# Kernel tuning notes

Hardware: AMD Instinct MI355X
Metric: run time of the kernel (lower is better)

The kernel has to match this reference:

```python
import jax, jax.numpy as jnp
import numpy as np
from jax.scipy.special import digamma

T, K, D = 8192, 64, 128


def setup_inputs() -> dict:
    key = jax.random.key(0)
    ks = jax.random.split(key, 7)
    mu_t = jax.random.normal(ks[0], (T, D), jnp.float32)
    diag_var_t = jax.random.uniform(ks[1], (T, D), jnp.float32)  # encoder diag variances >= 0
    niw_mu = jax.random.normal(ks[2], (K, D), jnp.float32)
    A = jax.random.normal(ks[3], (K, D, D), jnp.float32) / np.sqrt(D)
    niw_Psi = jnp.einsum('kde,kfe->kdf', A, A) + float(D) * jnp.eye(D, dtype=jnp.float32)[None]  # SPD
    niw_nu = D + 2.0 + 10.0 * jax.random.uniform(ks[4], (K,), jnp.float32)  # nu > D+1
    phi = 0.1 + 4.0 * jax.random.uniform(ks[5], (K, K), jnp.float32)  # Dirichlet posterior params > 0
    log_pi = jax.nn.log_softmax(jax.random.normal(ks[6], (K,), jnp.float32))
    return dict(mu_t=mu_t, diag_var_t=diag_var_t, niw_mu=niw_mu, niw_Psi=niw_Psi,
                niw_nu=niw_nu, phi=phi, log_pi=log_pi)


def _emission_logB(mu_t, diag_var_t, niw_mu, niw_Psi, niw_nu):
    # E[Lambda_k] = nu_k * Psi_k^{-1}; E[log|Lambda_k|] via multivariate digamma
    L = jnp.linalg.cholesky(niw_Psi)                                  # [K,D,D]
    logdet_Psi = 2.0 * jnp.sum(jnp.log(jnp.diagonal(L, axis1=-2, axis2=-1)), axis=-1)  # [K]
    eye = jnp.broadcast_to(jnp.eye(D, dtype=niw_Psi.dtype), (K, D, D))
    Psi_inv = jax.scipy.linalg.cho_solve((L, True), eye)              # [K,D,D]
    E_Lam = niw_nu[:, None, None] * Psi_inv                           # [K,D,D]
    i = jnp.arange(1, D + 1, dtype=niw_Psi.dtype)[None, :]            # [1,D]
    E_logdet = jnp.sum(digamma((niw_nu[:, None] + 1.0 - i) / 2.0), axis=1) \
        + D * jnp.log(jnp.asarray(2.0, niw_Psi.dtype)) - logdet_Psi   # [K]
    diagv = jnp.clip(diag_var_t, 0.0)                                 # [T,D]
    diff = mu_t[:, None, :] - niw_mu[None, :, :]                      # [T,K,D]
    quad_mean = jnp.einsum('tkd,kde,tke->tk', diff, E_Lam, diff)      # [T,K]
    ELam_diag = jnp.diagonal(E_Lam, axis1=-2, axis2=-1)               # [K,D]
    trace_diag = jnp.einsum('td,kd->tk', diagv, ELam_diag)            # [T,K]
    const = -0.5 * D * jnp.log(jnp.asarray(2.0 * np.pi, mu_t.dtype))
    return 0.5 * E_logdet[None, :] + const - 0.5 * (quad_mean + trace_diag)


def _forward_backward(log_pi, ElogA, logB):
    a0 = log_pi + logB[0]
    z0 = jax.nn.logsumexp(a0)
    alpha0 = a0 - z0

    def fwd_step(aprev, logb):
        pred = jax.nn.logsumexp(aprev[:, None] + ElogA, axis=0)
        a = pred + logb
        z = jax.nn.logsumexp(a)
        return a - z, (a - z, z)

    _, (alpha_rest, z_rest) = jax.lax.scan(fwd_step, alpha0, logB[1:])
    alpha = jnp.concatenate([alpha0[None], alpha_rest], axis=0)       # [T,K]
    logZ = jnp.concatenate([z0[None], z_rest], axis=0)                # [T]

    def bwd_step(bnext, xs):
        logb_next, z_next = xs
        b = jax.nn.logsumexp(ElogA + (logb_next + bnext)[None, :], axis=1) - z_next
        return b, b

    beta_T = jnp.zeros_like(alpha0)
    _, beta_rest = jax.lax.scan(bwd_step, beta_T, (logB[1:], logZ[1:]), reverse=True)
    beta = jnp.concatenate([beta_rest, beta_T[None]], axis=0)         # [T,K]

    rhat_log = alpha + beta
    rhat_log = rhat_log - jax.nn.logsumexp(rhat_log, axis=1, keepdims=True)
    rhat = jnp.exp(rhat_log)

    x = alpha[:-1, :, None] + ElogA[None, :, :] + (logB[1:] + beta[1:])[:, None, :]  # [T-1,K,K]
    x = x - jax.nn.logsumexp(x.reshape(x.shape[0], -1), axis=1)[:, None, None]
    xihat = jnp.exp(x)

    ll = jnp.sum(logZ)
    return rhat, xihat, ll


def reference(mu_t, diag_var_t, niw_mu, niw_Psi, niw_nu, phi, log_pi):
    logB = _emission_logB(mu_t, diag_var_t, niw_mu, niw_Psi, niw_nu)  # [T,K]
    ElogA = digamma(phi) - digamma(jnp.sum(phi, axis=1, keepdims=True))  # [K,K]
    rhat, xihat, ll = _forward_backward(log_pi, ElogA, logB)
    return rhat, xihat, ll
```

## Files before the change

kernel.cpp:

```cpp
#include <hip/hip_runtime.h>
#include <math.h>

#define T_LEN 8192
#define KK 64
#define DD 128
#define RS 132
#define GP 68

typedef __bf16  bf16x4 __attribute__((ext_vector_type(4)));
typedef __bf16  bf16x8 __attribute__((ext_vector_type(8)));
typedef float  f32x16 __attribute__((ext_vector_type(16)));

__device__ __forceinline__ float wred_max(float v){
#pragma unroll
  for (int m = 1; m < 64; m <<= 1) v = fmaxf(v, __shfl_xor(v, m, 64));
  return v;
}
__device__ __forceinline__ float wred_sum(float v){
#pragma unroll
  for (int m = 1; m < 64; m <<= 1) v += __shfl_xor(v, m, 64);
  return v;
}
__device__ __forceinline__ float digamma_f(float x){
  float r = 0.f;
  while (x < 6.f){ r -= 1.f/x; x += 1.f; }
  float ix = 1.f/x, ix2 = ix*ix;
  return r + logf(x) - 0.5f*ix - ix2*(0.0833333333f - ix2*(0.0083333333f - ix2*0.0039682540f));
}

__global__ void __launch_bounds__(256, 1) k_neumann(
    const float* __restrict__ Psi, const float* __restrict__ niw_mu,
    const float* __restrict__ nu_, const float* __restrict__ phi,
    __bf16* __restrict__ Ebf, float* __restrict__ EdiagT,
    float* __restrict__ cvecT, float* __restrict__ rK, float* __restrict__ Lhalf,
    float* __restrict__ sclK,
    float* __restrict__ ElogA, float* __restrict__ P, float* __restrict__ PT)
{
  extern __shared__ float lds[];
  float* Rl = lds;
  float* Pb = lds + DD*RS;
  __shared__ float red[256];
  __shared__ float msh[DD];
  int k = blockIdx.x, tid = threadIdx.x;
  const float* A = Psi + (size_t)k*DD*DD;

  if (tid < 64){
    float ph = phi[k*KK + tid];
    float s  = wred_sum(ph);
    float e  = digamma_f(ph) - digamma_f(s);
    ElogA[k*KK + tid] = e;
    float p = expf(e);
    P [k*KK + tid] = p;
    PT[tid*KK + k] = p;
  }

  float tl = 0.f;
  for (int d = tid; d < DD; d += 256) tl += A[d*DD + d];
  red[tid] = tl; __syncthreads();
  for (int off = 128; off > 0; off >>= 1){ if (tid < off) red[tid] += red[tid+off]; __syncthreads(); }
  float c = red[0] / (float)DD;
  __syncthreads();

  float trpow = 0.f;
  for (int idx = tid; idx < DD*DD; idx += 256){
    int d = idx >> 7, e = idx & 127;
    float v = ((d == e) ? 1.f : 0.f) - A[idx]/c;
    Rl[d*RS + e] = v;
    if (d == e) trpow += v;
  }
  __syncthreads();

  int tr = tid >> 4, tc = tid & 15;
  int r0 = tr*8, c0 = tc*8;
  float S[8][8];
#pragma unroll
  for (int i = 0; i < 8; i++)
#pragma unroll
    for (int j = 0; j < 8; j++){
      float v = Rl[(r0+i)*RS + c0+j];
      if (r0+i == c0+j) v += 1.f;
      S[i][j] = v;
    }

  {
    float Cc[8][8];
#pragma unroll
    for (int i = 0; i < 8; i++)
#pragma unroll
      for (int j = 0; j < 8; j++) Cc[i][j] = 0.f;
    for (int l = 0; l < DD; l += 4){
      float af[4][8], bf[4][8];
#pragma unroll
      for (int q = 0; q < 4; q++){
        float4 x0 = *(const float4*)&Rl[(l+q)*RS + r0];
        float4 x1 = *(const float4*)&Rl[(l+q)*RS + r0 + 4];
        af[q][0]=x0.x; af[q][1]=x0.y; af[q][2]=x0.z; af[q][3]=x0.w;
        af[q][4]=x1.x; af[q][5]=x1.y; af[q][6]=x1.z; af[q][7]=x1.w;
        float4 y0 = *(const float4*)&Rl[(l+q)*RS + c0];
        float4 y1 = *(const float4*)&Rl[(l+q)*RS + c0 + 4];
        bf[q][0]=y0.x; bf[q][1]=y0.y; bf[q][2]=y0.z; bf[q][3]=y0.w;
        bf[q][4]=y1.x; bf[q][5]=y1.y; bf[q][6]=y1.z; bf[q][7]=y1.w;
      }
#pragma unroll
      for (int q = 0; q < 4; q++)
#pragma unroll
        for (int i = 0; i < 8; i++)
#pragma unroll
          for (int j = 0; j < 8; j++)
            Cc[i][j] = fmaf(af[q][i], bf[q][j], Cc[i][j]);
    }
#pragma unroll
    for (int i = 0; i < 8; i++)
#pragma unroll
      for (int j = 0; j < 8; j++) S[i][j] += Cc[i][j];
    if (tr == tc){
#pragma unroll
      for (int i = 0; i < 8; i++) trpow += Cc[i][i]*0.5f;
    }
  }

  red[tid] = trpow; __syncthreads();
  for (int off = 128; off > 0; off >>= 1){ if (tid < off) red[tid] += red[tid+off]; __syncthreads(); }
  float trsum = red[0];
  __syncthreads();

  float nu = nu_[k];
  float dl = 0.f;
  for (int i = tid; i < DD; i += 256) dl += digamma_f((nu - (float)i)*0.5f);
  red[tid] = dl; __syncthreads();
  for (int off = 128; off > 0; off >>= 1){ if (tid < off) red[tid] += red[tid+off]; __syncthreads(); }
  if (tid == 0){
    float logdetPsi = (float)DD*logf(c) - trsum;
    float Elogdet = red[0] + (float)DD*0.69314718056f - logdetPsi;
    Lhalf[k] = 0.5f*Elogdet - 0.5f*(float)DD*1.83787706641f;
    sclK[k]  = nu / c;
  }
  __syncthreads();

  float scl = nu / c;
#pragma unroll
  for (int i = 0; i < 8; i++)
#pragma unroll
    for (int j = 0; j < 8; j++){
      float sv = S[i][j];
      bool dg = (r0+i == c0+j);
      if (dg) EdiagT[(r0+i)*KK + k] = scl*sv;
      float et = scl*(sv - (dg ? 1.f : 0.f));
      int r = (r0+i)*DD + (c0+j);
      Ebf[(size_t)(r>>4)*1024 + k*16 + (r&15)] = (__bf16)et;
    }
#pragma unroll
  for (int i = 0; i < 8; i++){
    float4 w0, w1;
    w0.x=S[i][0]; w0.y=S[i][1]; w0.z=S[i][2]; w0.w=S[i][3];
    w1.x=S[i][4]; w1.y=S[i][5]; w1.z=S[i][6]; w1.w=S[i][7];
    *(float4*)&Pb[(r0+i)*RS + c0]     = w0;
    *(float4*)&Pb[(r0+i)*RS + c0 + 4] = w1;
  }
  for (int d = tid; d < DD; d += 256) msh[d] = niw_mu[k*DD + d];
  __syncthreads();
  float cv = 0.f;
  if (tid < DD){
    float acc = 0.f;
    for (int e = 0; e < DD; e++) acc += Pb[tid*RS + e]*msh[e];
    cv = scl*acc;
    cvecT[tid*KK + k] = cv;
  }
  red[tid] = (tid < DD) ? msh[tid]*cv : 0.f; __syncthreads();
  for (int off = 128; off > 0; off >>= 1){ if (tid < off) red[tid] += red[tid+off]; __syncthreads(); }
  if (tid == 0) rK[k] = red[0];
}

__global__ void __launch_bounds__(256, 1) k_q1(const float* __restrict__ mu,
      const __bf16* __restrict__ Ebf, float* __restrict__ part)
{
  __shared__ float muF[32*132];
  __shared__ float trb[128*66];
  int b = blockIdx.x;
  int rs = b & 3, tseg = b >> 2;
  int t0 = tseg*128, d0 = rs*32;
  int tid = threadIdx.x;
  int w = tid >> 6, lane = tid & 63;
  int kh = w & 1, th = w >> 1;
  int l31 = lane & 31;
  int k0 = (lane >> 5)*8;

  for (int v = tid; v < 128*32; v += 256){
    int t = v >> 5, d = v & 31;
    muF[d*132 + t] = mu[(size_t)(t0+t)*DD + d0 + d];
  }

  bf16x8 Bf0[8], Bf1[8];
#pragma unroll
  for (int c = 0; c < 8; c++){
    int tc0 = t0 + th*64 + l31;
    int tc1 = tc0 + 32;
    float4 x0 = *(const float4*)&mu[(size_t)tc0*DD + c*16 + k0];
    float4 x1 = *(const float4*)&mu[(size_t)tc0*DD + c*16 + k0 + 4];
    bf16x8 hv;
    hv[0]=(__bf16)x0.x; hv[1]=(__bf16)x0.y; hv[2]=(__bf16)x0.z; hv[3]=(__bf16)x0.w;
    hv[4]=(__bf16)x1.x; hv[5]=(__bf16)x1.y; hv[6]=(__bf16)x1.z; hv[7]=(__bf16)x1.w;
    Bf0[c] = hv;
    float4 y0 = *(const float4*)&mu[(size_t)tc1*DD + c*16 + k0];
    float4 y1 = *(const float4*)&mu[(size_t)tc1*DD + c*16 + k0 + 4];
    bf16x8 gv;
    gv[0]=(__bf16)y0.x; gv[1]=(__bf16)y0.y; gv[2]=(__bf16)y0.z; gv[3]=(__bf16)y0.w;
    gv[4]=(__bf16)y1.x; gv[5]=(__bf16)y1.y; gv[6]=(__bf16)y1.z; gv[7]=(__bf16)y1.w;
    Bf1[c] = gv;
  }
  __syncthreads();

  const unsigned short* __restrict__ Eu = (const unsigned short*)Ebf;
  size_t abase = (size_t)(kh*32 + l31)*16 + k0;

  f32x16 acc0, acc1;
#pragma unroll
  for (int i = 0; i < 16; i++){ acc0[i]=0.f; acc1[i]=0.f; }

  uint4 A0[8], A1[8];
  {
    const unsigned short* ap = Eu + (size_t)d0*8192 + abase;
#pragma unroll
    for (int c = 0; c < 8; c++) A0[c] = *(const uint4*)(ap + c*1024);
#pragma unroll
    for (int c = 0; c < 8; c++) A1[c] = *(const uint4*)(ap + 8192 + c*1024);
  }

  for (int dd = 0; dd < 32; dd += 2){
    {
      f32x16 ta, tb;
#pragma unroll
      for (int i = 0; i < 16; i++){ ta[i]=0.f; tb[i]=0.f; }
#pragma unroll
      for (int c = 0; c < 8; c++){
        bf16x8 av = *(bf16x8*)&A0[c];
        ta = __builtin_amdgcn_mfma_f32_32x32x16_bf16(av, Bf0[c], ta, 0, 0, 0);
        tb = __builtin_amdgcn_mfma_f32_32x32x16_bf16(av, Bf1[c], tb, 0, 0, 0);
      }
      float m0 = muF[dd*132 + th*64 + l31];
      float m1 = muF[dd*132 + th*64 + 32 + l31];
#pragma unroll
      for (int i = 0; i < 16; i++){
        acc0[i] = fmaf(m0, ta[i], acc0[i]);
        acc1[i] = fmaf(m1, tb[i], acc1[i]);
      }
    }
    if (dd + 2 < 32){
      const unsigned short* ap = Eu + (size_t)(d0+dd+2)*8192 + abase;
#pragma unroll
      for (int c = 0; c < 8; c++) A0[c] = *(const uint4*)(ap + c*1024);
    }
    {
      f32x16 ta, tb;
#pragma unroll
      for (int i = 0; i < 16; i++){ ta[i]=0.f; tb[i]=0.f; }
#pragma unroll
      for (int c = 0; c < 8; c++){
        bf16x8 av = *(bf16x8*)&A1[c];
        ta = __builtin_amdgcn_mfma_f32_32x32x16_bf16(av, Bf0[c], ta, 0, 0, 0);
        tb = __builtin_amdgcn_mfma_f32_32x32x16_bf16(av, Bf1[c], tb, 0, 0, 0);
      }
      float m0 = muF[(dd+1)*132 + th*64 + l31];
      float m1 = muF[(dd+1)*132 + th*64 + 32 + l31];
#pragma unroll
      for (int i = 0; i < 16; i++){
        acc0[i] = fmaf(m0, ta[i], acc0[i]);
        acc1[i] = fmaf(m1, tb[i], acc1[i]);
      }
    }
    if (dd + 3 < 32){
      const unsigned short* ap = Eu + (size_t)(d0+dd+3)*8192 + abase;
#pragma unroll
      for (int c = 0; c < 8; c++) A1[c] = *(const uint4*)(ap + c*1024);
    }
  }

  __syncthreads();
#pragma unroll
  for (int r = 0; r < 16; r++){
    int krow = kh*32 + (r&3) + 8*(r>>2) + 4*(lane>>5);
    trb[(th*64 + l31)*66 + krow]      = acc0[r];
    trb[(th*64 + 32 + l31)*66 + krow] = acc1[r];
  }
  __syncthreads();
  float* dst = part + (size_t)rs*T_LEN*KK;
  {
    int t = tid >> 1, kc = (tid & 1)*32;
#pragma unroll
    for (int q = 0; q < 8; q++){
      float4 vv = *(float4*)&trb[t*66 + kc + q*4];
      *(float4*)&dst[(size_t)(t0+t)*KK + kc + q*4] = vv;
    }
  }
}

__global__ void __launch_bounds__(256) k_logBall(
    const float* __restrict__ part, const float* __restrict__ mu, const float* __restrict__ dvar,
    const float* __restrict__ cvecT, const float* __restrict__ EdiagT,
    const float* __restrict__ rK, const float* __restrict__ Lhalf, const float* __restrict__ sclK,
    float* __restrict__ logB, float* __restrict__ mrow, float* __restrict__ btil)
{
  int tid = threadIdx.x; int k = tid & 63; int w = tid >> 6;
  float rk = rK[k], lh = Lhalf[k], scl = sclK[k];
  int tbase = blockIdx.x*32 + w*8;
  float a1[8], a2[8], ssv[8];
#pragma unroll
  for (int tt = 0; tt < 8; tt++){ a1[tt]=0.f; a2[tt]=0.f; ssv[tt]=0.f; }
  for (int dc = 0; dc < DD; dc += 4){
    float c0 = cvecT[(dc+0)*KK + k], c1 = cvecT[(dc+1)*KK + k];
    float c2 = cvecT[(dc+2)*KK + k], c3 = cvecT[(dc+3)*KK + k];
    float e0 = EdiagT[(dc+0)*KK + k], e1 = EdiagT[(dc+1)*KK + k];
    float e2 = EdiagT[(dc+2)*KK + k], e3 = EdiagT[(dc+3)*KK + k];
#pragma unroll
    for (int tt = 0; tt < 8; tt++){
      float4 m4 = *(const float4*)(mu   + (size_t)(tbase+tt)*DD + dc);
      float4 v4 = *(const float4*)(dvar + (size_t)(tbase+tt)*DD + dc);
      a1[tt] = fmaf(m4.x,c0, fmaf(m4.y,c1, fmaf(m4.z,c2, fmaf(m4.w,c3, a1[tt]))));
      a2[tt] = fmaf(fmaxf(v4.x,0.f),e0, fmaf(fmaxf(v4.y,0.f),e1,
               fmaf(fmaxf(v4.z,0.f),e2, fmaf(fmaxf(v4.w,0.f),e3, a2[tt]))));
      ssv[tt] = fmaf(m4.x,m4.x, fmaf(m4.y,m4.y, fmaf(m4.z,m4.z, fmaf(m4.w,m4.w, ssv[tt]))));
    }
  }
#pragma unroll
  for (int tt = 0; tt < 8; tt++){
    int t = tbase + tt;
    float q = scl*ssv[tt]
            + part[(size_t)0*T_LEN*KK + (size_t)t*KK + k]
            + part[(size_t)1*T_LEN*KK + (size_t)t*KK + k]
            + part[(size_t)2*T_LEN*KK + (size_t)t*KK + k]
            + part[(size_t)3*T_LEN*KK + (size_t)t*KK + k];
    float lb = lh - 0.5f*(q - 2.f*a1[tt] + rk + a2[tt]);
    float m  = wred_max(lb);
    logB[(size_t)t*KK + k] = lb;
    btil[(size_t)t*KK + k] = expf(lb - m);
    if (k == 0) mrow[t] = m;
  }
}

__global__ void __launch_bounds__(128, 1) k_pass1(const float* __restrict__ Pm,
     const float* __restrict__ btil, float* __restrict__ G8)
{
  __shared__ float G[64*GP];
  __shared__ float wmax[2][2];
  int tid = threadIdx.x, w = tid >> 6, lane = tid & 63;
  int chunk = blockIdx.x;
  int kb8 = (lane >> 5)*8;
  int n = lane & 31;

  bf16x8 Bhi[4][2], Blo[4][2];
#pragma unroll
  for (int Kb = 0; Kb < 4; Kb++)
#pragma unroll
    for (int J = 0; J < 2; J++){
#pragma unroll
      for (int j = 0; j < 8; j++){
        float p = Pm[(Kb*16 + kb8 + j)*KK + J*32 + n];
        __bf16 h = (__bf16)p;
        Bhi[Kb][J][j] = h;
        Blo[Kb][J][j] = (__bf16)(p - (float)h);
      }
    }
  for (int v = tid; v < 64*64; v += 128){
    int i = v >> 6, j = v & 63;
    G[i*GP + j] = (i == j) ? 1.f : 0.f;
  }
  __syncthreads();

  int m = w*32 + n;
  for (int s = 0; s < 8; s++){
    int t = chunk*8 + s;
    if (t >= 1){
      f32x16 acc0, acc1;
#pragma unroll
      for (int i = 0; i < 16; i++){ acc0[i] = 0.f; acc1[i] = 0.f; }
#pragma unroll
      for (int Kb = 0; Kb < 4; Kb++){
        float4 x0 = *(const float4*)&G[m*GP + Kb*16 + kb8];
        float4 x1 = *(const float4*)&G[m*GP + Kb*16 + kb8 + 4];
        float xv[8] = {x0.x,x0.y,x0.z,x0.w,x1.x,x1.y,x1.z,x1.w};
        bf16x8 ah, al;
#pragma unroll
        for (int j = 0; j < 8; j++){
          __bf16 h = (__bf16)xv[j];
          ah[j] = h;
          al[j] = (__bf16)(xv[j] - (float)h);
        }
        acc0 = __builtin_amdgcn_mfma_f32_32x32x16_bf16(ah, Bhi[Kb][0], acc0, 0,0,0);
        acc0 = __builtin_amdgcn_mfma_f32_32x32x16_bf16(ah, Blo[Kb][0], acc0, 0,0,0);
        acc0 = __builtin_amdgcn_mfma_f32_32x32x16_bf16(al, Bhi[Kb][0], acc0, 0,0,0);
        acc1 = __builtin_amdgcn_mfma_f32_32x32x16_bf16(ah, Bhi[Kb][1], acc1, 0,0,0);
        acc1 = __builtin_amdgcn_mfma_f32_32x32x16_bf16(ah, Blo[Kb][1], acc1, 0,0,0);
        acc1 = __builtin_amdgcn_mfma_f32_32x32x16_bf16(al, Bhi[Kb][1], acc1, 0,0,0);
      }
      float b0 = btil[(size_t)t*KK + n];
      float b1 = btil[(size_t)t*KK + 32 + n];
      float mx = 0.f;
#pragma unroll
      for (int i = 0; i < 16; i++){
        acc0[i] *= b0; acc1[i] *= b1;
        mx = fmaxf(mx, fmaxf(acc0[i], acc1[i]));
      }
      mx = wred_max(mx);
      if (lane == 0) wmax[s&1][w] = mx;
      __syncthreads();
      float inv = 1.f/fmaxf(wmax[s&1][0], wmax[s&1][1]);
#pragma unroll
      for (int r = 0; r < 16; r++){
        int row = w*32 + (r&3) + 8*(r>>2) + 4*(lane>>5);
        G[row*GP + n]      = acc0[r]*inv;
        G[row*GP + 32 + n] = acc1[r]*inv;
      }
    }
  }
  __syncthreads();
  float* dst = G8 + (size_t)chunk*4096;
  for (int v = tid; v < 4096; v += 128) dst[v] = G[(v>>6)*GP + (v&63)];
}

__device__ void chain_body(const float* __restrict__ s0, int chain,
    float* __restrict__ X, float (*wmax)[2],
    float* __restrict__ dstLin, int tid, int w, int lane)
{
  int kb8 = (lane >> 5)*8;
  int n = lane & 31;
  int m = w*32 + n;

  for (int v = tid; v < 4096; v += 128) X[(v>>6)*GP + (v&63)] = s0[v];
  __syncthreads();

  for (int j = 1; j < chain; j++){
    const float* Y = s0 + (size_t)j*4096;
    bf16x8 Bh[4][2], Bl[4][2];
#pragma unroll
    for (int Kb = 0; Kb < 4; Kb++)
#pragma unroll
      for (int J = 0; J < 2; J++){
#pragma unroll
        for (int jj = 0; jj < 8; jj++){
          float p = Y[(Kb*16 + kb8 + jj)*64 + J*32 + n];
          __bf16 h = (__bf16)p;
          Bh[Kb][J][jj] = h;
          Bl[Kb][J][jj] = (__bf16)(p - (float)h);
        }
      }
    f32x16 acc0, acc1;
#pragma unroll
    for (int i = 0; i < 16; i++){ acc0[i] = 0.f; acc1[i] = 0.f; }
#pragma unroll
    for (int Kb = 0; Kb < 4; Kb++){
      float4 x0 = *(const float4*)&X[m*GP + Kb*16 + kb8];
      float4 x1 = *(const float4*)&X[m*GP + Kb*16 + kb8 + 4];
      float xv[8] = {x0.x,x0.y,x0.z,x0.w,x1.x,x1.y,x1.z,x1.w};
      bf16x8 ah, al;
#pragma unroll
      for (int q = 0; q < 8; q++){
        __bf16 h = (__bf16)xv[q];
        ah[q] = h;
        al[q] = (__bf16)(xv[q] - (float)h);
      }
      acc0 = __builtin_amdgcn_mfma_f32_32x32x16_bf16(ah, Bh[Kb][0], acc0, 0,0,0);
      acc0 = __builtin_amdgcn_mfma_f32_32x32x16_bf16(ah, Bl[Kb][0], acc0, 0,0,0);
      acc0 = __builtin_amdgcn_mfma_f32_32x32x16_bf16(al, Bh[Kb][0], acc0, 0,0,0);
      acc1 = __builtin_amdgcn_mfma_f32_32x32x16_bf16(ah, Bh[Kb][1], acc1, 0,0,0);
      acc1 = __builtin_amdgcn_mfma_f32_32x32x16_bf16(ah, Bl[Kb][1], acc1, 0,0,0);
      acc1 = __builtin_amdgcn_mfma_f32_32x32x16_bf16(al, Bh[Kb][1], acc1, 0,0,0);
    }
    float mx = 0.f;
#pragma unroll
    for (int i = 0; i < 16; i++) mx = fmaxf(mx, fmaxf(acc0[i], acc1[i]));
    mx = wred_max(mx);
    if (lane == 0) wmax[j&1][w] = mx;
    __syncthreads();
    float inv = 1.f/fmaxf(wmax[j&1][0], wmax[j&1][1]);
#pragma unroll
    for (int r = 0; r < 16; r++){
      int row = w*32 + (r&3) + 8*(r>>2) + 4*(lane>>5);
      X[row*GP + n]      = acc0[r]*inv;
      X[row*GP + 32 + n] = acc1[r]*inv;
    }
    __syncthreads();
  }
  for (int v = tid; v < 4096; v += 128) dstLin[v] = X[(v>>6)*GP + (v&63)];
}

__global__ void __launch_bounds__(128, 1) k_chain8(const float* __restrict__ G8,
        float* __restrict__ H64)
{
  __shared__ float X[64*GP];
  __shared__ float wmax[2][2];
  int tid = threadIdx.x, w = tid >> 6, lane = tid & 63;
  int bid = blockIdx.x;
  chain_body(G8 + (size_t)bid*8*4096, 8, X, wmax, H64 + (size_t)bid*4096, tid, w, lane);
}

__device__ void mat_combine(const float* __restrict__ A, const float* __restrict__ B,
    float* __restrict__ out, float* __restrict__ outT,
    float* __restrict__ X, float* __restrict__ wmax, int tid, int w, int lane)
{
  int kb8 = (lane >> 5)*8;
  int n = lane & 31;
  int m = w*32 + n;
  for (int v = tid; v < 4096; v += 128) X[(v>>6)*GP + (v&63)] = A[v];
  bf16x8 Bh[4][2], Bl[4][2];
#pragma unroll
  for (int Kb = 0; Kb < 4; Kb++)
#pragma unroll
    for (int J = 0; J < 2; J++){
#pragma unroll
      for (int jj = 0; jj < 8; jj++){
        float p = B[(Kb*16 + kb8 + jj)*64 + J*32 + n];
        __bf16 h = (__bf16)p;
        Bh[Kb][J][jj] = h;
        Bl[Kb][J][jj] = (__bf16)(p - (float)h);
      }
    }
  __syncthreads();
  f32x16 acc0, acc1;
#pragma unroll
  for (int i = 0; i < 16; i++){ acc0[i] = 0.f; acc1[i] = 0.f; }
#pragma unroll
  for (int Kb = 0; Kb < 4; Kb++){
    float4 x0 = *(const float4*)&X[m*GP + Kb*16 + kb8];
    float4 x1 = *(const float4*)&X[m*GP + Kb*16 + kb8 + 4];
    float xv[8] = {x0.x,x0.y,x0.z,x0.w,x1.x,x1.y,x1.z,x1.w};
    bf16x8 ah, al;
#pragma unroll
    for (int q = 0; q < 8; q++){
      __bf16 h = (__bf16)xv[q];
      ah[q] = h;
      al[q] = (__bf16)(xv[q] - (float)h);
    }
    acc0 = __builtin_amdgcn_mfma_f32_32x32x16_bf16(ah, Bh[Kb][0], acc0, 0,0,0);
    acc0 = __builtin_amdgcn_mfma_f32_32x32x16_bf16(ah, Bl[Kb][0], acc0, 0,0,0);
    acc0 = __builtin_amdgcn_mfma_f32_32x32x16_bf16(al, Bh[Kb][0], acc0, 0,0,0);
    acc1 = __builtin_amdgcn_mfma_f32_32x32x16_bf16(ah, Bh[Kb][1], acc1, 0,0,0);
    acc1 = __builtin_amdgcn_mfma_f32_32x32x16_bf16(ah, Bl[Kb][1], acc1, 0,0,0);
    acc1 = __builtin_amdgcn_mfma_f32_32x32x16_bf16(al, Bh[Kb][1], acc1, 0,0,0);
  }
  float mx = 0.f;
#pragma unroll
  for (int i = 0; i < 16; i++) mx = fmaxf(mx, fmaxf(acc0[i], acc1[i]));
  mx = wred_max(mx);
  if (lane == 0) wmax[w] = mx;
  __syncthreads();
  float inv = 1.f/fmaxf(wmax[0], wmax[1]);
#pragma unroll
  for (int r = 0; r < 16; r++){
    int row = w*32 + (r&3) + 8*(r>>2) + 4*(lane>>5);
    out[row*64 + n]      = acc0[r]*inv;
    out[row*64 + 32 + n] = acc1[r]*inv;
  }
  if (outT){
    __syncthreads();
#pragma unroll
    for (int r = 0; r < 16; r++){
      int row = w*32 + (r&3) + 8*(r>>2) + 4*(lane>>5);
      X[row*GP + n]      = acc0[r]*inv;
      X[row*GP + 32 + n] = acc1[r]*inv;
    }
    __syncthreads();
    for (int v = tid; v < 4096; v += 128) outT[v] = X[(v&63)*GP + (v>>6)];
  }
}

__device__ void mat_copy(const float* __restrict__ A, float* __restrict__ out,
    float* __restrict__ outT, float* __restrict__ X, int tid)
{
  if (!outT){
    for (int v = tid; v < 4096; v += 128) out[v] = A[v];
  } else {
    for (int v = tid; v < 4096; v += 128){
      float vv = A[v];
      out[v] = vv;
      X[(v>>6)*GP + (v&63)] = vv;
    }
    __syncthreads();
    for (int v = tid; v < 4096; v += 128) outT[v] = X[(v&63)*GP + (v>>6)];
  }
}

__global__ void __launch_bounds__(128, 1) k_ks(
    const float* __restrict__ PAin, float* __restrict__ PAout,
    const float* __restrict__ SBin, float* __restrict__ SBout,
    float* __restrict__ SBT, int s, int wrT)
{
  __shared__ float X[64*GP];
  __shared__ float wmax[2];
  int tid = threadIdx.x, w = tid >> 6, lane = tid & 63;
  int c = blockIdx.x;
  if (c >= s)
    mat_combine(PAin + (size_t)(c-s)*4096, PAin + (size_t)c*4096,
                PAout + (size_t)c*4096, nullptr, X, wmax, tid, w, lane);
  else
    mat_copy(PAin + (size_t)c*4096, PAout + (size_t)c*4096, nullptr, X, tid);
  __syncthreads();
  float* t = wrT ? (SBT + (size_t)c*4096) : nullptr;
  if (c + s <= 127)
    mat_combine(SBin + (size_t)c*4096, SBin + (size_t)(c+s)*4096,
                SBout + (size_t)c*4096, t, X, wmax, tid, w, lane);
  else
    mat_copy(SBin + (size_t)c*4096, SBout + (size_t)c*4096, t, X, tid);
}

__global__ void __launch_bounds__(64, 1) k_pass3(const float* __restrict__ Pm, const float* __restrict__ PTm,
   const float* __restrict__ PA, const float* __restrict__ SBT,
   const float* __restrict__ logB, const float* __restrict__ mrow, const float* __restrict__ btil,
   const float* __restrict__ log_pi,
   float* __restrict__ alphahat, float* __restrict__ betahat, float* __restrict__ llpart)
{
  int lane = threadIdx.x;
  int bid = blockIdx.x;
  if (bid < 128){
    int c = bid;
    float Preg[64];
#pragma unroll
    for (int i = 0; i < 64; i++) Preg[i] = Pm[i*64 + lane];
    float a; float llacc = 0.f;
    int tstart;
    float x0v = log_pi[lane] + logB[lane];
    float mm0 = wred_max(x0v);
    float e0 = expf(x0v - mm0);
    float ss0 = wred_sum(e0);
    if (c == 0){
      a = e0/ss0;
      llacc = mm0 + logf(ss0);
      alphahat[lane] = a;
      tstart = 1;
    } else {
      float a0 = e0/ss0;
      const float* H = PA + (size_t)(c-1)*4096;
      float Hr[64];
#pragma unroll
      for (int i = 0; i < 64; i++) Hr[i] = H[i*64 + lane];
      float p0 = 0.f, p1 = 0.f, p2 = 0.f, p3 = 0.f;
#pragma unroll
      for (int i = 0; i < 16; i++){
        p0 = fmaf(__shfl(a0, i,      64), Hr[i],      p0);
        p1 = fmaf(__shfl(a0, i + 16, 64), Hr[i + 16], p1);
        p2 = fmaf(__shfl(a0, i + 32, 64), Hr[i + 32], p2);
        p3 = fmaf(__shfl(a0, i + 48, 64), Hr[i + 48], p3);
      }
      a = (p0 + p1) + (p2 + p3);
      a /= wred_sum(a);
      tstart = c*64;
    }
    int tend = c*64 + 64;
    float bt = btil[(size_t)tstart*KK + lane];
    for (int t = tstart; t < tend; t++){
      float btn = 0.f;
      if (t + 1 < tend) btn = btil[(size_t)(t+1)*KK + lane];
      float mr = mrow[t];
      float p0 = 0.f, p1 = 0.f, p2 = 0.f, p3 = 0.f;
#pragma unroll
      for (int i = 0; i < 16; i++){
        p0 = fmaf(__shfl(a, i,      64), Preg[i],      p0);
        p1 = fmaf(__shfl(a, i + 16, 64), Preg[i + 16], p1);
        p2 = fmaf(__shfl(a, i + 32, 64), Preg[i + 32], p2);
        p3 = fmaf(__shfl(a, i + 48, 64), Preg[i + 48], p3);
      }
      float pred = (p0 + p1) + (p2 + p3);
      a = pred * bt;
      if (((t - tstart) & 3) == 3 || t == tend - 1){
        float s = wred_sum(a);
        a = a / s;
        llacc += logf(s);
      }
      llacc += mr;
      alphahat[(size_t)t*KK + lane] = a;
      bt = btn;
    }
    if (lane == 0) llpart[c] = llacc;
  } else {
    int c = bid - 128;
    float PTreg[64];
#pragma unroll
    for (int j = 0; j < 64; j++) PTreg[j] = PTm[j*64 + lane];
    float b, lb;
    if (c == 127){
      b = 1.f; lb = 0.f;
    } else {
      const float* H = SBT + (size_t)(c+1)*4096;
      float s0 = 0.f, s1 = 0.f, s2 = 0.f, s3 = 0.f;
#pragma unroll
      for (int i = 0; i < 16; i++){
        s0 += H[(i     )*64 + lane];
        s1 += H[(i + 16)*64 + lane];
        s2 += H[(i + 32)*64 + lane];
        s3 += H[(i + 48)*64 + lane];
      }
      float s = (s0 + s1) + (s2 + s3);
      float mmb = wred_max(s);
      b = s/mmb;
      lb = logf(b);
    }
    int t1 = c*64 + 63;
    betahat[(size_t)t1*KK + lane] = b;
    float lgb = logB[(size_t)t1*KK + lane];
    float mrn = mrow[t1];
    for (int t = t1 - 1; t >= c*64; t--){
      float lgbn = 0.f, mrnn = 0.f;
      if (t > c*64){
        lgbn = logB[(size_t)t*KK + lane];
        mrnn = mrow[t];
      }
      float lv = (lgb - mrn) + lb;
      float vm = wred_max(lv);
      float vv = expf(lv - vm);
      float q0 = 0.f, q1r = 0.f, q2 = 0.f, q3 = 0.f;
#pragma unroll
      for (int j = 0; j < 16; j++){
        q0  = fmaf(PTreg[j],      __shfl(vv, j,      64), q0);
        q1r = fmaf(PTreg[j + 16], __shfl(vv, j + 16, 64), q1r);
        q2  = fmaf(PTreg[j + 32], __shfl(vv, j + 32, 64), q2);
        q3  = fmaf(PTreg[j + 48], __shfl(vv, j + 48, 64), q3);
      }
      b = (q0 + q1r) + (q2 + q3);
      lb = logf(b);
      betahat[(size_t)t*KK + lane] = b;
      lgb = lgbn; mrn = mrnn;
    }
  }
}

__global__ void __launch_bounds__(256) k_outs(const float* __restrict__ ah,
     const float* __restrict__ bh, const float* __restrict__ ElogA,
     const float* __restrict__ logB, const float* __restrict__ llp,
     float* __restrict__ out_rhat, float* __restrict__ out_xi, float* __restrict__ out_ll)
{
  __shared__ float la[64], wc[64];
  __shared__ float redm[4], reds[4];
  int tid = threadIdx.x;
  int b = blockIdx.x;
  if (tid < 64) la[tid] = logf(ah[(size_t)b*KK + tid]);
  else if (tid < 128 && b < T_LEN-1){
    int j = tid - 64;
    wc[j] = logB[(size_t)(b+1)*KK + j] + logf(bh[(size_t)(b+1)*KK + j]);
  }
  __syncthreads();
  if (tid < 64){
    float s = la[tid] + logf(bh[(size_t)b*KK + tid]);
    float m = wred_max(s);
    float p = (m < -3.0e37f) ? 1.f : expf(s - m);
    float ss = wred_sum(p);
    out_rhat[(size_t)b*KK + tid] = p/ss;
  }
  if (b == T_LEN-1){
    if (tid >= 64 && tid < 128){
      int i = tid - 64;
      float v = llp[i] + llp[i + 64];
      v = wred_sum(v);
      if (i == 0) out_ll[0] = v;
    }
    return;
  }
  int lane = tid & 63, w = tid >> 6;
  int j0 = (lane & 15) << 2;
  int ibase = w*16 + (lane >> 4)*4;
  float4 wc4 = *(float4*)&wc[j0];
  float sv[16];
  float mx = -3.0e38f;
#pragma unroll
  for (int ii = 0; ii < 4; ii++){
    float lai = la[ibase + ii];
    float4 e4 = *(const float4*)&ElogA[(ibase+ii)*KK + j0];
    float s0 = lai + e4.x + wc4.x;
    float s1 = lai + e4.y + wc4.y;
    float s2 = lai + e4.z + wc4.z;
    float s3 = lai + e4.w + wc4.w;
    sv[ii*4+0]=s0; sv[ii*4+1]=s1; sv[ii*4+2]=s2; sv[ii*4+3]=s3;
    mx = fmaxf(fmaxf(fmaxf(mx, s0), fmaxf(s1, s2)), s3);
  }
  float mxw = wred_max(mx);
  if (lane == 0) redm[w] = mxw;
  __syncthreads();
  float m = fmaxf(fmaxf(redm[0], redm[1]), fmaxf(redm[2], redm[3]));
  bool degen = !(m > -3.0e37f);
  float pv[16]; float ps = 0.f;
#pragma unroll
  for (int n = 0; n < 16; n++){
    float p = degen ? 1.f : expf(sv[n] - m);
    pv[n] = p; ps += p;
  }
  float psw = wred_sum(ps);
  if (lane == 0) reds[w] = psw;
  __syncthreads();
  float inv = 1.f/(reds[0] + reds[1] + reds[2] + reds[3]);
  float* dst = out_xi + (size_t)b*4096;
#pragma unroll
  for (int ii = 0; ii < 4; ii++){
    float4 o;
    o.x = pv[ii*4+0]*inv; o.y = pv[ii*4+1]*inv;
    o.z = pv[ii*4+2]*inv; o.w = pv[ii*4+3]*inv;
    *(float4*)&dst[(ibase+ii)*KK + j0] = o;
  }
}

extern "C" void kernel_launch(void* const* d_in, const int* in_sizes, int n_in,
                              void* d_out, int out_size, void* d_ws, size_t ws_size,
                              hipStream_t stream)
{
  const float* mu    = (const float*)d_in[0];
  const float* dvar  = (const float*)d_in[1];
  const float* niwmu = (const float*)d_in[2];
  const float* Psi   = (const float*)d_in[3];
  const float* nu    = (const float*)d_in[4];
  const float* phi   = (const float*)d_in[5];
  const float* lpi   = (const float*)d_in[6];
  float* out = (float*)d_out;
  float* ws  = (float*)d_ws;

  size_t o = 0;
  float* EbfF   = ws + o; o += (size_t)DD*DD*KK/2;
  float* EdiagT = ws + o; o += (size_t)DD*KK;
  float* cvecT  = ws + o; o += (size_t)DD*KK;
  float* rK     = ws + o; o += KK;
  float* Lhalf  = ws + o; o += KK;
  float* sclK   = ws + o; o += KK;
  float* ElogA  = ws + o; o += KK*KK;
  float* P      = ws + o; o += KK*KK;
  float* PT     = ws + o; o += KK*KK;
  float* logB   = ws + o; o += (size_t)T_LEN*KK;
  float* mrowp  = ws + o; o += T_LEN;
  float* btil   = ws + o; o += (size_t)T_LEN*KK;
  float* G8     = ws + o; o += (size_t)1024*4096;
  float* H64    = ws + o; o += (size_t)128*4096;
  float* llp    = ws + o; o += 128;
  float* ah     = ws + o; o += (size_t)T_LEN*KK;
  float* bh     = ws + o; o += (size_t)T_LEN*KK;
  if (ws_size < o*sizeof(float)) return;

  __bf16* Ebf = (__bf16*)EbfF;
  float*  part = G8;

  const size_t M = (size_t)128*4096;
  float* PAa = G8;
  float* PAb = G8 + M;
  float* SBa = G8 + 2*M;
  float* SBb = G8 + 3*M;
  float* SBT = G8 + 4*M;

  hipFuncSetAttribute((const void*)k_neumann, hipFuncAttributeMaxDynamicSharedMemorySize, 2*DD*RS*4);

  k_neumann<<<64, 256, 2*DD*RS*4, stream>>>(Psi, niwmu, nu, phi, Ebf, EdiagT, cvecT, rK, Lhalf, sclK, ElogA, P, PT);
  k_q1<<<256, 256, 0, stream>>>(mu, Ebf, part);
  k_logBall<<<256, 256, 0, stream>>>(part, mu, dvar, cvecT, EdiagT, rK, Lhalf, sclK, logB, mrowp, btil);
  k_pass1<<<1024, 128, 0, stream>>>(P, btil, G8);
  k_chain8<<<128, 128, 0, stream>>>(G8, H64);
  k_ks<<<128, 128, 0, stream>>>(H64, PAb, H64, SBb, SBT,  1, 0);
  k_ks<<<128, 128, 0, stream>>>(PAb, PAa, SBb, SBa, SBT,  2, 0);
  k_ks<<<128, 128, 0, stream>>>(PAa, PAb, SBa, SBb, SBT,  4, 0);
  k_ks<<<128, 128, 0, stream>>>(PAb, PAa, SBb, SBa, SBT,  8, 0);
  k_ks<<<128, 128, 0, stream>>>(PAa, PAb, SBa, SBb, SBT, 16, 0);
  k_ks<<<128, 128, 0, stream>>>(PAb, PAa, SBb, SBa, SBT, 32, 0);
  k_ks<<<128, 128, 0, stream>>>(PAa, PAb, SBa, SBb, SBT, 64, 1);
  k_pass3<<<256, 64, 0, stream>>>(P, PT, PAb, SBT, logB, mrowp, btil, lpi, ah, bh, llp);
  k_outs<<<T_LEN, 256, 0, stream>>>(ah, bh, ElogA, logB, llp, out, out + (size_t)T_LEN*KK,
                                    out + (size_t)T_LEN*KK + (size_t)(T_LEN-1)*KK*KK);
}
```

Measured before the change: 430.5 us.

## Replace Kogge-Stone matrix scan with two-level chunk products and sequential vector propagation

The 8-step pass1, the chain8 kernel and seven Kogge-Stone combine launches are replaced by three stages. Per-32-step transfer matrices (and their transposes) are built in 256 blocks, and 16 blocks multiply these into 16 super-matrices. The forward and backward blocks then propagate their boundary vectors sequentially with matrix-vector products over super and per-32 matrices. This removes many kernel launches and the log-depth matrix-matrix products, but each pass3 block now does up to about 30 serial 64x64 mat-vecs with global loads, and pass32 runs 32 serial steps per block.

```diff
diff --git a/kernel.cpp b/kernel.cpp
--- a/kernel.cpp
+++ b/kernel.cpp
@@ -337,8 +337,8 @@
   }
 }
 
-__global__ void __launch_bounds__(128, 1) k_pass1(const float* __restrict__ Pm,
-     const float* __restrict__ btil, float* __restrict__ G8)
+__global__ void __launch_bounds__(128, 1) k_pass32(const float* __restrict__ Pm,
+     const float* __restrict__ btil, float* __restrict__ H32, float* __restrict__ H32T)
 {
   __shared__ float G[64*GP];
   __shared__ float wmax[2][2];
@@ -367,8 +367,8 @@
   __syncthreads();
 
   int m = w*32 + n;
-  for (int s = 0; s < 8; s++){
-    int t = chunk*8 + s;
+  for (int s = 0; s < 32; s++){
+    int t = chunk*32 + s;
     if (t >= 1){
       f32x16 acc0, acc1;
 #pragma unroll
@@ -410,11 +410,13 @@
         G[row*GP + n]      = acc0[r]*inv;
         G[row*GP + 32 + n] = acc1[r]*inv;
       }
-    }
-  }
-  __syncthreads();
-  float* dst = G8 + (size_t)chunk*4096;
+      __syncthreads();
+    }
+  }
+  float* dst = H32 + (size_t)chunk*4096;
   for (int v = tid; v < 4096; v += 128) dst[v] = G[(v>>6)*GP + (v&63)];
+  float* dstT = H32T + (size_t)chunk*4096;
+  for (int v = tid; v < 4096; v += 128) dstT[v] = G[(v&63)*GP + (v>>6)];
 }
 
 __device__ void chain_body(const float* __restrict__ s0, int chain,
@@ -483,133 +485,39 @@
   for (int v = tid; v < 4096; v += 128) dstLin[v] = X[(v>>6)*GP + (v&63)];
 }
 
-__global__ void __launch_bounds__(128, 1) k_chain8(const float* __restrict__ G8,
-        float* __restrict__ H64)
+__global__ void __launch_bounds__(128, 1) k_super(const float* __restrict__ H32,
+        float* __restrict__ S, float* __restrict__ ST)
 {
   __shared__ float X[64*GP];
   __shared__ float wmax[2][2];
   int tid = threadIdx.x, w = tid >> 6, lane = tid & 63;
-  int bid = blockIdx.x;
-  chain_body(G8 + (size_t)bid*8*4096, 8, X, wmax, H64 + (size_t)bid*4096, tid, w, lane);
-}
-
-__device__ void mat_combine(const float* __restrict__ A, const float* __restrict__ B,
-    float* __restrict__ out, float* __restrict__ outT,
-    float* __restrict__ X, float* __restrict__ wmax, int tid, int w, int lane)
-{
-  int kb8 = (lane >> 5)*8;
-  int n = lane & 31;
-  int m = w*32 + n;
-  for (int v = tid; v < 4096; v += 128) X[(v>>6)*GP + (v&63)] = A[v];
-  bf16x8 Bh[4][2], Bl[4][2];
-#pragma unroll
-  for (int Kb = 0; Kb < 4; Kb++)
-#pragma unroll
-    for (int J = 0; J < 2; J++){
-#pragma unroll
-      for (int jj = 0; jj < 8; jj++){
-        float p = B[(Kb*16 + kb8 + jj)*64 + J*32 + n];
-        __bf16 h = (__bf16)p;
-        Bh[Kb][J][jj] = h;
-        Bl[Kb][J][jj] = (__bf16)(p - (float)h);
-      }
-    }
-  __syncthreads();
-  f32x16 acc0, acc1;
-#pragma unroll
-  for (int i = 0; i < 16; i++){ acc0[i] = 0.f; acc1[i] = 0.f; }
-#pragma unroll
-  for (int Kb = 0; Kb < 4; Kb++){
-    float4 x0 = *(const float4*)&X[m*GP + Kb*16 + kb8];
-    float4 x1 = *(const float4*)&X[m*GP + Kb*16 + kb8 + 4];
-    float xv[8] = {x0.x,x0.y,x0.z,x0.w,x1.x,x1.y,x1.z,x1.w};
-    bf16x8 ah, al;
-#pragma unroll
-    for (int q = 0; q < 8; q++){
-      __bf16 h = (__bf16)xv[q];
-      ah[q] = h;
-      al[q] = (__bf16)(xv[q] - (float)h);
-    }
-    acc0 = __builtin_amdgcn_mfma_f32_32x32x16_bf16(ah, Bh[Kb][0], acc0, 0,0,0);
-    acc0 = __builtin_amdgcn_mfma_f32_32x32x16_bf16(ah, Bl[Kb][0], acc0, 0,0,0);
-    acc0 = __builtin_amdgcn_mfma_f32_32x32x16_bf16(al, Bh[Kb][0], acc0, 0,0,0);
-    acc1 = __builtin_amdgcn_mfma_f32_32x32x16_bf16(ah, Bh[Kb][1], acc1, 0,0,0);
-    acc1 = __builtin_amdgcn_mfma_f32_32x32x16_bf16(ah, Bl[Kb][1], acc1, 0,0,0);
-    acc1 = __builtin_amdgcn_mfma_f32_32x32x16_bf16(al, Bh[Kb][1], acc1, 0,0,0);
-  }
-  float mx = 0.f;
-#pragma unroll
-  for (int i = 0; i < 16; i++) mx = fmaxf(mx, fmaxf(acc0[i], acc1[i]));
-  mx = wred_max(mx);
-  if (lane == 0) wmax[w] = mx;
-  __syncthreads();
-  float inv = 1.f/fmaxf(wmax[0], wmax[1]);
-#pragma unroll
-  for (int r = 0; r < 16; r++){
-    int row = w*32 + (r&3) + 8*(r>>2) + 4*(lane>>5);
-    out[row*64 + n]      = acc0[r]*inv;
-    out[row*64 + 32 + n] = acc1[r]*inv;
-  }
-  if (outT){
-    __syncthreads();
-#pragma unroll
-    for (int r = 0; r < 16; r++){
-      int row = w*32 + (r&3) + 8*(r>>2) + 4*(lane>>5);
-      X[row*GP + n]      = acc0[r]*inv;
-      X[row*GP + 32 + n] = acc1[r]*inv;
-    }
-    __syncthreads();
-    for (int v = tid; v < 4096; v += 128) outT[v] = X[(v&63)*GP + (v>>6)];
-  }
-}
-
-__device__ void mat_copy(const float* __restrict__ A, float* __restrict__ out,
-    float* __restrict__ outT, float* __restrict__ X, int tid)
-{
-  if (!outT){
-    for (int v = tid; v < 4096; v += 128) out[v] = A[v];
-  } else {
-    for (int v = tid; v < 4096; v += 128){
-      float vv = A[v];
-      out[v] = vv;
-      X[(v>>6)*GP + (v&63)] = vv;
-    }
-    __syncthreads();
-    for (int v = tid; v < 4096; v += 128) outT[v] = X[(v&63)*GP + (v>>6)];
-  }
-}
-
-__global__ void __launch_bounds__(128, 1) k_ks(
-    const float* __restrict__ PAin, float* __restrict__ PAout,
-    const float* __restrict__ SBin, float* __restrict__ SBout,
-    float* __restrict__ SBT, int s, int wrT)
-{
-  __shared__ float X[64*GP];
-  __shared__ float wmax[2];
-  int tid = threadIdx.x, w = tid >> 6, lane = tid & 63;
-  int c = blockIdx.x;
-  if (c >= s)
-    mat_combine(PAin + (size_t)(c-s)*4096, PAin + (size_t)c*4096,
-                PAout + (size_t)c*4096, nullptr, X, wmax, tid, w, lane);
-  else
-    mat_copy(PAin + (size_t)c*4096, PAout + (size_t)c*4096, nullptr, X, tid);
-  __syncthreads();
-  float* t = wrT ? (SBT + (size_t)c*4096) : nullptr;
-  if (c + s <= 127)
-    mat_combine(SBin + (size_t)c*4096, SBin + (size_t)(c+s)*4096,
-                SBout + (size_t)c*4096, t, X, wmax, tid, w, lane);
-  else
-    mat_copy(SBin + (size_t)c*4096, SBout + (size_t)c*4096, t, X, tid);
-}
-
-__global__ void __launch_bounds__(64, 1) k_pass3(const float* __restrict__ Pm, const float* __restrict__ PTm,
-   const float* __restrict__ PA, const float* __restrict__ SBT,
+  int j = blockIdx.x;
+  chain_body(H32 + (size_t)j*16*4096, 16, X, wmax, S + (size_t)j*4096, tid, w, lane);
+  __syncthreads();
+  float* dstT = ST + (size_t)j*4096;
+  for (int v = tid; v < 4096; v += 128) dstT[v] = X[(v&63)*GP + (v>>6)];
+}
+
+#define P2_LOAD(H, base, cc) do { const float* g_ = (base) + (size_t)(cc)*4096; \
+  _Pragma("unroll") for (int i_ = 0; i_ < 64; i_++) H[i_] = g_[i_*64 + lane]; } while(0)
+#define P2_STEP_NN(H, v) do { float p0_=0.f,p1_=0.f,p2_=0.f,p3_=0.f; \
+  _Pragma("unroll") for (int i_ = 0; i_ < 16; i_++){ \
+    p0_ = fmaf(__shfl(v, i_,      64), H[i_],      p0_); \
+    p1_ = fmaf(__shfl(v, i_ + 16, 64), H[i_ + 16], p1_); \
+    p2_ = fmaf(__shfl(v, i_ + 32, 64), H[i_ + 32], p2_); \
+    p3_ = fmaf(__shfl(v, i_ + 48, 64), H[i_ + 48], p3_); } \
+  v = (p0_ + p1_) + (p2_ + p3_); } while(0)
+
+__global__ void __launch_bounds__(64, 1) k_pass3p(const float* __restrict__ Pm, const float* __restrict__ PTm,
+   const float* __restrict__ H32, const float* __restrict__ H32T,
+   const float* __restrict__ Sup, const float* __restrict__ SupT,
    const float* __restrict__ logB, const float* __restrict__ mrow, const float* __restrict__ btil,
    const float* __restrict__ log_pi,
    float* __restrict__ alphahat, float* __restrict__ betahat, float* __restrict__ llpart)
 {
   int lane = threadIdx.x;
   int bid = blockIdx.x;
+  float Hr[64];
   if (bid < 128){
     int c = bid;
     float Preg[64];
@@ -627,21 +535,19 @@
       alphahat[lane] = a;
       tstart = 1;
     } else {
-      float a0 = e0/ss0;
-      const float* H = PA + (size_t)(c-1)*4096;
-      float Hr[64];
-#pragma unroll
-      for (int i = 0; i < 64; i++) Hr[i] = H[i*64 + lane];
-      float p0 = 0.f, p1 = 0.f, p2 = 0.f, p3 = 0.f;
-#pragma unroll
-      for (int i = 0; i < 16; i++){
-        p0 = fmaf(__shfl(a0, i,      64), Hr[i],      p0);
-        p1 = fmaf(__shfl(a0, i + 16, 64), Hr[i + 16], p1);
-        p2 = fmaf(__shfl(a0, i + 32, 64), Hr[i + 32], p2);
-        p3 = fmaf(__shfl(a0, i + 48, 64), Hr[i + 48], p3);
-      }
-      a = (p0 + p1) + (p2 + p3);
-      a /= wred_sum(a);
+      float v = e0/ss0;
+      int q = (2*c) >> 4;
+      for (int jj = 0; jj < q; jj++){
+        P2_LOAD(Hr, Sup, jj);
+        P2_STEP_NN(Hr, v);
+        v /= wred_sum(v);
+      }
+      for (int jj = 16*q; jj < 2*c; jj++){
+        P2_LOAD(Hr, H32, jj);
+        P2_STEP_NN(Hr, v);
+        v /= wred_sum(v);
+      }
+      a = v;
       tstart = c*64;
     }
     int tend = c*64 + 64;
@@ -679,18 +585,20 @@
     if (c == 127){
       b = 1.f; lb = 0.f;
     } else {
-      const float* H = SBT + (size_t)(c+1)*4096;
-      float s0 = 0.f, s1 = 0.f, s2 = 0.f, s3 = 0.f;
-#pragma unroll
-      for (int i = 0; i < 16; i++){
-        s0 += H[(i     )*64 + lane];
-        s1 += H[(i + 16)*64 + lane];
-        s2 += H[(i + 32)*64 + lane];
-        s3 += H[(i + 48)*64 + lane];
-      }
-      float s = (s0 + s1) + (s2 + s3);
-      float mmb = wred_max(s);
-      b = s/mmb;
+      float v = 1.f;
+      int start = 2*c + 2;
+      int m0 = (start + 15) >> 4;
+      for (int jj = 15; jj >= m0; jj--){
+        P2_LOAD(Hr, SupT, jj);
+        P2_STEP_NN(Hr, v);
+        v /= wred_max(v);
+      }
+      for (int jj = 16*m0 - 1; jj >= start; jj--){
+        P2_LOAD(Hr, H32T, jj);
+        P2_STEP_NN(Hr, v);
+        v /= wred_max(v);
+      }
+      b = v;
       lb = logf(b);
     }
     int t1 = c*64 + 63;
@@ -822,38 +730,26 @@
   float* logB   = ws + o; o += (size_t)T_LEN*KK;
   float* mrowp  = ws + o; o += T_LEN;
   float* btil   = ws + o; o += (size_t)T_LEN*KK;
-  float* G8     = ws + o; o += (size_t)1024*4096;
-  float* H64    = ws + o; o += (size_t)128*4096;
+  float* part   = ws + o; o += (size_t)4*T_LEN*KK;
+  float* H32    = ws + o; o += (size_t)256*4096;
+  float* H32T   = ws + o; o += (size_t)256*4096;
+  float* Sup    = ws + o; o += (size_t)16*4096;
+  float* SupT   = ws + o; o += (size_t)16*4096;
   float* llp    = ws + o; o += 128;
   float* ah     = ws + o; o += (size_t)T_LEN*KK;
   float* bh     = ws + o; o += (size_t)T_LEN*KK;
   if (ws_size < o*sizeof(float)) return;
 
   __bf16* Ebf = (__bf16*)EbfF;
-  float*  part = G8;
-
-  const size_t M = (size_t)128*4096;
-  float* PAa = G8;
-  float* PAb = G8 + M;
-  float* SBa = G8 + 2*M;
-  float* SBb = G8 + 3*M;
-  float* SBT = G8 + 4*M;
 
   hipFuncSetAttribute((const void*)k_neumann, hipFuncAttributeMaxDynamicSharedMemorySize, 2*DD*RS*4);
 
   k_neumann<<<64, 256, 2*DD*RS*4, stream>>>(Psi, niwmu, nu, phi, Ebf, EdiagT, cvecT, rK, Lhalf, sclK, ElogA, P, PT);
   k_q1<<<256, 256, 0, stream>>>(mu, Ebf, part);
   k_logBall<<<256, 256, 0, stream>>>(part, mu, dvar, cvecT, EdiagT, rK, Lhalf, sclK, logB, mrowp, btil);
-  k_pass1<<<1024, 128, 0, stream>>>(P, btil, G8);
-  k_chain8<<<128, 128, 0, stream>>>(G8, H64);
-  k_ks<<<128, 128, 0, stream>>>(H64, PAb, H64, SBb, SBT,  1, 0);
-  k_ks<<<128, 128, 0, stream>>>(PAb, PAa, SBb, SBa, SBT,  2, 0);
-  k_ks<<<128, 128, 0, stream>>>(PAa, PAb, SBa, SBb, SBT,  4, 0);
-  k_ks<<<128, 128, 0, stream>>>(PAb, PAa, SBb, SBa, SBT,  8, 0);
-  k_ks<<<128, 128, 0, stream>>>(PAa, PAb, SBa, SBb, SBT, 16, 0);
-  k_ks<<<128, 128, 0, stream>>>(PAb, PAa, SBb, SBa, SBT, 32, 0);
-  k_ks<<<128, 128, 0, stream>>>(PAa, PAb, SBa, SBb, SBT, 64, 1);
-  k_pass3<<<256, 64, 0, stream>>>(P, PT, PAb, SBT, logB, mrowp, btil, lpi, ah, bh, llp);
+  k_pass32<<<256, 128, 0, stream>>>(P, btil, H32, H32T);
+  k_super<<<16, 128, 0, stream>>>(H32, Sup, SupT);
+  k_pass3p<<<256, 64, 0, stream>>>(P, PT, H32, H32T, Sup, SupT, logB, mrowp, btil, lpi, ah, bh, llp);
   k_outs<<<T_LEN, 256, 0, stream>>>(ah, bh, ElogA, logB, llp, out, out + (size_t)T_LEN*KK,
                                     out + (size_t)T_LEN*KK + (size_t)(T_LEN-1)*KK*KK);
 }
```

Measured after the change: 425.7 us. About the same (-1.1%).
